# Kernel optimization log

Measured on AMD Instinct MI355X. Metric: run time of the kernel, lower is better.

The kernel has to match this reference:

```python
import jax, jax.numpy as jnp
import numpy as np

N_NODES = 50000
N_EDGES = 800000
D = 128
R = 8


def setup_inputs() -> dict:
    key = jax.random.key(0)
    ks = jax.random.split(key, 8)
    x = jax.random.normal(ks[0], (N_NODES, D), dtype=jnp.float32)
    edge_index = jax.random.randint(ks[1], (2, N_EDGES), 0, N_NODES, dtype=jnp.int64)
    edge_type = jax.random.randint(ks[2], (N_EDGES,), 0, R, dtype=jnp.int64)
    scale = 0.02
    W1 = jax.random.normal(ks[3], (R, D, D), dtype=jnp.float32) * scale
    root1 = jax.random.normal(ks[4], (D, D), dtype=jnp.float32) * scale
    b1 = jnp.zeros((D,), dtype=jnp.float32)
    W2 = jax.random.normal(ks[5], (R, D, D), dtype=jnp.float32) * scale
    root2 = jax.random.normal(ks[6], (D, D), dtype=jnp.float32) * scale
    b2 = jnp.zeros((D,), dtype=jnp.float32)
    return {"x": x, "edge_index": edge_index, "edge_type": edge_type,
            "W1": W1, "root1": root1, "b1": b1,
            "W2": W2, "root2": root2, "b2": b2}


def rgcn_conv(x, src, dst, etype, W, root, b):
    """PyG RGCNConv: per-relation mean aggregation + root transform + bias."""
    n = x.shape[0]
    out = x @ root + b  # [N, O]
    num_rel = W.shape[0]
    for r in range(num_rel):  # small fixed relation count
        m = (etype == r).astype(x.dtype)  # [E] relation mask as weight
        y = x @ W[r]  # [N, O] transform once per relation
        msg = y[src] * m[:, None]  # [E, O] gathered, masked messages
        s = jax.ops.segment_sum(msg, dst, num_segments=n)
        cnt = jax.ops.segment_sum(m, dst, num_segments=n)
        out = out + s / jnp.clip(cnt, 1.0)[:, None]
    return out


def reference(x, edge_index, edge_type, W1, root1, b1, W2, root2, b2):
    src, dst = edge_index[0], edge_index[1]
    h = rgcn_conv(x, src, dst, edge_type, W1, root1, b1)
    h = jax.nn.relu(h)
    h = rgcn_conv(h, src, dst, edge_type, W2, root2, b2)
    # F.normalize(h, dim=-1): x / max(||x||_2, eps)
    norm = jnp.linalg.norm(h, axis=-1, keepdims=True)
    return h / jnp.maximum(norm, 1e-12)
```

## Files before the change

### kernel.cpp

```cpp
#include <hip/hip_runtime.h>

#define NN 50000
#define NE 800000
#define DD 128
#define RR 8
#define MB (NN * RR)
#define SCAN_BLK 2048
#define NBLK ((MB + SCAN_BLK - 1) / SCAN_BLK)

typedef __attribute__((ext_vector_type(8))) short short8;
typedef __attribute__((ext_vector_type(4))) float f32x4;

__device__ __forceinline__ unsigned short f2bf(float f)
{
    unsigned int u = __float_as_uint(f);
    u = (u + 0x7FFFu + ((u >> 16) & 1u)) >> 16;
    return (unsigned short)u;
}
__device__ __forceinline__ float bflo(unsigned int p) { return __uint_as_float(p << 16); }
__device__ __forceinline__ float bfhi(unsigned int p) { return __uint_as_float(p & 0xFFFF0000u); }

__global__ __launch_bounds__(256) void k_count(const int* __restrict__ ei,
                                               const int* __restrict__ et,
                                               int* __restrict__ cnt)
{
    int e = blockIdx.x * 256 + threadIdx.x;
    if (e < NE) {
        int r = et[e];
        int dst = ei[NE + e];
        atomicAdd(&cnt[r * NN + dst], 1);
    }
}

__global__ __launch_bounds__(256) void k_scan1(const int* __restrict__ cnt,
                                               int* __restrict__ off,
                                               int* __restrict__ bsum)
{
    __shared__ int lds[256];
    int t = threadIdx.x;
    int base = blockIdx.x * SCAN_BLK + t * 8;
    int v[8], s = 0;
    #pragma unroll
    for (int j = 0; j < 8; j++) {
        int idx = base + j;
        v[j] = (idx < MB) ? cnt[idx] : 0;
        s += v[j];
    }
    lds[t] = s;
    __syncthreads();
    for (int d = 1; d < 256; d <<= 1) {
        int u = (t >= d) ? lds[t - d] : 0;
        __syncthreads();
        lds[t] += u;
        __syncthreads();
    }
    if (t == 255) bsum[blockIdx.x] = lds[255];
    int run = lds[t] - s;
    #pragma unroll
    for (int j = 0; j < 8; j++) {
        int idx = base + j;
        if (idx < MB) off[idx] = run;
        run += v[j];
    }
}

__global__ __launch_bounds__(256) void k_scan2(const int* __restrict__ bsum,
                                               int* __restrict__ carry)
{
    __shared__ int lds[256];
    int t = threadIdx.x;
    int s = (t < NBLK) ? bsum[t] : 0;
    lds[t] = s;
    __syncthreads();
    for (int d = 1; d < 256; d <<= 1) {
        int u = (t >= d) ? lds[t - d] : 0;
        __syncthreads();
        lds[t] += u;
        __syncthreads();
    }
    if (t < NBLK) carry[t] = lds[t] - s;
}

__global__ __launch_bounds__(256) void k_scan3(int* __restrict__ off,
                                               const int* __restrict__ carry)
{
    int c = carry[blockIdx.x];
    int base = blockIdx.x * SCAN_BLK + threadIdx.x * 8;
    #pragma unroll
    for (int j = 0; j < 8; j++) {
        int idx = base + j;
        if (idx < MB) off[idx] += c;
    }
    if (blockIdx.x == 0 && threadIdx.x == 0) off[MB] = NE;
}

__global__ __launch_bounds__(256) void k_place(const int* __restrict__ ei,
                                               const int* __restrict__ et,
                                               const int* __restrict__ off,
                                               int* __restrict__ fill,
                                               int* __restrict__ srt)
{
    int e = blockIdx.x * 256 + threadIdx.x;
    if (e < NE) {
        int r = et[e];
        int src = ei[e];
        int dst = ei[NE + e];
        int b = r * NN + dst;
        int pos = off[b] + atomicAdd(&fill[b], 1);
        srt[pos] = src;
    }
}

__global__ __launch_bounds__(256) void k_tobf16(const float* __restrict__ x,
                                                unsigned short* __restrict__ xb, int n4)
{
    int i = blockIdx.x * 256 + threadIdx.x;
    if (i < n4) {
        float4 v = ((const float4*)x)[i];
        uint2 o;
        o.x = (unsigned int)f2bf(v.x) | ((unsigned int)f2bf(v.y) << 16);
        o.y = (unsigned int)f2bf(v.z) | ((unsigned int)f2bf(v.w) << 16);
        ((uint2*)xb)[i] = o;
    }
}

__global__ __launch_bounds__(256) void k_wconv(const float* __restrict__ W1,
                                               const float* __restrict__ root1,
                                               const float* __restrict__ W2,
                                               const float* __restrict__ root2,
                                               unsigned short* __restrict__ Wb)
{
    int e = blockIdx.x * 256 + threadIdx.x;
    if (e >= 18 * 16384) return;
    int m = e >> 14;
    int rem = e & 16383;
    int n = rem >> 7;
    int k = rem & 127;
    float v;
    if (m < 8)       v = W1[m * 16384 + k * 128 + n];
    else if (m == 8) v = root1[k * 128 + n];
    else if (m < 17) v = W2[(m - 9) * 16384 + k * 128 + n];
    else             v = root2[k * 128 + n];
    Wb[e] = f2bf(v);
}

__global__ __launch_bounds__(512) void k_layer(const unsigned short* __restrict__ Xin,
                                               const unsigned short* __restrict__ Wb,
                                               const float* __restrict__ bias,
                                               const int* __restrict__ off,
                                               const int* __restrict__ srt,
                                               unsigned short* __restrict__ out_bf,
                                               float* __restrict__ out_f,
                                               int mode)
{
    __shared__ unsigned short Wl[128 * 128];
    __shared__ unsigned short Al[64 * 128];
    const int t = threadIdx.x;
    const int w = t >> 6;
    const int lane = t & 63;
    const int grow0 = blockIdx.x * 64;
    const int colb = lane & 15;
    const int hi = lane >> 4;
    const int g = t >> 4;
    const int l16 = t & 15;

    const int arow = ((w >> 1) << 4) + colb;
    const int aswz = (arow & 7) << 4;

    f32x4 acc[4];
    #pragma unroll
    for (int tt = 0; tt < 4; tt++) acc[tt] = f32x4{0.f, 0.f, 0.f, 0.f};

    for (int m = 0; m < 9; m++) {
        {
            const uint4* wsrc = (const uint4*)(Wb + (size_t)m * 16384);
            #pragma unroll
            for (int c = 0; c < 4; c++) {
                int u = c * 512 + t;
                uint4 v = wsrc[u];
                int n = u >> 4;
                int dstb = (u * 16) ^ ((n & 7) << 4);
                *(uint4*)((char*)Wl + dstb) = v;
            }
        }
        if (m < 8) {
            int b0 = m * NN + grow0;
            #pragma unroll
            for (int rr = 0; rr < 2; rr++) {
                int row = g * 2 + rr;
                int dstn = grow0 + row;
                float a0 = 0.f, a1 = 0.f, a2 = 0.f, a3 = 0.f;
                float a4 = 0.f, a5 = 0.f, a6 = 0.f, a7 = 0.f;
                int c = 0;
                if (dstn < NN) {
                    int s0 = off[b0 + row];
                    int s1 = off[b0 + row + 1];
                    c = s1 - s0;
                    for (int k = 0; k < c; k++) {
                        int src = srt[s0 + k];
                        uint4 u = *(const uint4*)(Xin + (size_t)src * 128 + l16 * 8);
                        a0 += bflo(u.x); a1 += bfhi(u.x);
                        a2 += bflo(u.y); a3 += bfhi(u.y);
                        a4 += bflo(u.z); a5 += bfhi(u.z);
                        a6 += bflo(u.w); a7 += bfhi(u.w);
                    }
                }
                float invc = 1.0f / (float)(c > 1 ? c : 1);
                uint4 o;
                o.x = (unsigned int)f2bf(a0 * invc) | ((unsigned int)f2bf(a1 * invc) << 16);
                o.y = (unsigned int)f2bf(a2 * invc) | ((unsigned int)f2bf(a3 * invc) << 16);
                o.z = (unsigned int)f2bf(a4 * invc) | ((unsigned int)f2bf(a5 * invc) << 16);
                o.w = (unsigned int)f2bf(a6 * invc) | ((unsigned int)f2bf(a7 * invc) << 16);
                int byteoff = (row * 256 + l16 * 16) ^ ((row & 7) << 4);
                *(uint4*)((char*)Al + byteoff) = o;
            }
        }
        __syncthreads();

        if (m < 8) {
            #pragma unroll
            for (int ks = 0; ks < 4; ks++) {
                int abyte = (arow * 256 + ks * 64 + hi * 16) ^ aswz;
                short8 af = *(const short8*)((const char*)Al + abyte);
                #pragma unroll
                for (int tt = 0; tt < 4; tt++) {
                    int n = (w & 1) * 64 + tt * 16 + colb;
                    int bbyte = (n * 256 + ks * 64 + hi * 16) ^ ((n & 7) << 4);
                    short8 bfr = *(const short8*)((const char*)Wl + bbyte);
                    acc[tt] = __builtin_amdgcn_mfma_f32_16x16x32_bf16(af, bfr, acc[tt], 0, 0, 0);
                }
            }
        } else {
            int rowg = grow0 + arow;
            #pragma unroll
            for (int ks = 0; ks < 4; ks++) {
                short8 af = short8{0,0,0,0,0,0,0,0};
                if (rowg < NN)
                    af = *(const short8*)(Xin + (size_t)rowg * 128 + ks * 32 + hi * 8);
                #pragma unroll
                for (int tt = 0; tt < 4; tt++) {
                    int n = (w & 1) * 64 + tt * 16 + colb;
                    int bbyte = (n * 256 + ks * 64 + hi * 16) ^ ((n & 7) << 4);
                    short8 bfr = *(const short8*)((const char*)Wl + bbyte);
                    acc[tt] = __builtin_amdgcn_mfma_f32_16x16x32_bf16(af, bfr, acc[tt], 0, 0, 0);
                }
            }
        }
        __syncthreads();
    }

    const int rl_base = (w >> 1) << 4;
    if (mode == 0) {
        #pragma unroll
        for (int tt = 0; tt < 4; tt++) {
            int col = (w & 1) * 64 + tt * 16 + colb;
            float bc = bias[col];
            #pragma unroll
            for (int j = 0; j < 4; j++) {
                int row = grow0 + rl_base + hi * 4 + j;
                if (row < NN) {
                    float v = fmaxf(acc[tt][j] + bc, 0.f);
                    out_bf[(size_t)row * 128 + col] = f2bf(v);
                }
            }
        }
    } else {
        float vv[4][4];
        float ss[4] = {0.f, 0.f, 0.f, 0.f};
        #pragma unroll
        for (int tt = 0; tt < 4; tt++) {
            int col = (w & 1) * 64 + tt * 16 + colb;
            float bc = bias[col];
            #pragma unroll
            for (int j = 0; j < 4; j++) {
                float v = acc[tt][j] + bc;
                vv[tt][j] = v;
                ss[j] += v * v;
            }
        }
        #pragma unroll
        for (int j = 0; j < 4; j++) {
            #pragma unroll
            for (int o = 1; o < 16; o <<= 1) ss[j] += __shfl_xor(ss[j], o);
        }
        float* nrm = (float*)Al;
        if (colb == 0) {
            #pragma unroll
            for (int j = 0; j < 4; j++) nrm[(rl_base + hi * 4 + j) * 2 + (w & 1)] = ss[j];
        }
        __syncthreads();
        #pragma unroll
        for (int tt = 0; tt < 4; tt++) {
            int col = (w & 1) * 64 + tt * 16 + colb;
            #pragma unroll
            for (int j = 0; j < 4; j++) {
                int rl = rl_base + hi * 4 + j;
                int row = grow0 + rl;
                if (row < NN) {
                    float tot = nrm[rl * 2] + nrm[rl * 2 + 1];
                    float inv = 1.0f / fmaxf(sqrtf(tot), 1e-12f);
                    out_f[(size_t)row * 128 + col] = vv[tt][j] * inv;
                }
            }
        }
    }
}

extern "C" void kernel_launch(void* const* d_in, const int* in_sizes, int n_in,
                              void* d_out, int out_size, void* d_ws, size_t ws_size,
                              hipStream_t stream)
{
    const float* x     = (const float*)d_in[0];
    const int*   ei    = (const int*)d_in[1];
    const int*   et    = (const int*)d_in[2];
    const float* W1    = (const float*)d_in[3];
    const float* root1 = (const float*)d_in[4];
    const float* b1    = (const float*)d_in[5];
    const float* W2    = (const float*)d_in[6];
    const float* root2 = (const float*)d_in[7];
    const float* b2    = (const float*)d_in[8];
    float* out = (float*)d_out;

    char* ws = (char*)d_ws;
    int* cnt   = (int*)ws;
    int* fill  = cnt + MB;
    int* off   = fill + MB;
    int* bsum  = off + MB + 1;
    int* carry = bsum + 256;
    int* srt   = carry + 256;
    unsigned short* Xb = (unsigned short*)(srt + NE);
    unsigned short* hb = Xb + (size_t)NN * DD;
    unsigned short* Wb = hb + (size_t)NN * DD;

    hipMemsetAsync(cnt, 0, (size_t)2 * MB * 4, stream);

    k_count<<<(NE + 255) / 256, 256, 0, stream>>>(ei, et, cnt);
    k_scan1<<<NBLK, 256, 0, stream>>>(cnt, off, bsum);
    k_scan2<<<1, 256, 0, stream>>>(bsum, carry);
    k_scan3<<<NBLK, 256, 0, stream>>>(off, carry);
    k_place<<<(NE + 255) / 256, 256, 0, stream>>>(ei, et, off, fill, srt);

    k_tobf16<<<(NN * DD / 4 + 255) / 256, 256, 0, stream>>>(x, Xb, NN * DD / 4);
    k_wconv<<<(18 * 16384 + 255) / 256, 256, 0, stream>>>(W1, root1, W2, root2, Wb);

    int lay_grid = (NN + 63) / 64;
    k_layer<<<lay_grid, 512, 0, stream>>>(Xb, Wb, b1, off, srt, hb, nullptr, 0);
    k_layer<<<lay_grid, 512, 0, stream>>>(hb, Wb + (size_t)9 * 16384, b2, off, srt, nullptr, out, 1);
}
```

Measured before the change: 379.2 us.

## Hoist all-relation neighbor gather before GEMM loop with 32-row tiles

The layer kernel now gathers and sums neighbor features for all 8 relations up front into registers (64 floats per thread), with the loads unrolled by two. The gather no longer sits between weight staging and MFMA inside each relation iteration. The row tile shrinks from 64 to 32 so each thread handles one destination row. Each wave now covers 16 rows by 32 columns, and the grid doubles. The aim is more memory-level parallelism in the random gathers and fewer sync-serialized gather phases. The cost is higher register pressure, and each block reloads the 9 weight matrices for only 32 rows, doubling LDS weight traffic per row.

```diff
diff --git a/kernel.cpp b/kernel.cpp
--- a/kernel.cpp
+++ b/kernel.cpp
@@ -154,23 +154,69 @@
                                                int mode)
 {
     __shared__ unsigned short Wl[128 * 128];
-    __shared__ unsigned short Al[64 * 128];
+    __shared__ unsigned short Al[32 * 128];
     const int t = threadIdx.x;
     const int w = t >> 6;
     const int lane = t & 63;
-    const int grow0 = blockIdx.x * 64;
+    const int grow0 = blockIdx.x * 32;
     const int colb = lane & 15;
     const int hi = lane >> 4;
     const int g = t >> 4;
     const int l16 = t & 15;
 
-    const int arow = ((w >> 1) << 4) + colb;
+    const int rt = w & 1;
+    const int ct0 = w >> 1;
+    const int arow = rt * 16 + colb;
     const int aswz = (arow & 7) << 4;
 
-    f32x4 acc[4];
-    #pragma unroll
-    for (int tt = 0; tt < 4; tt++) acc[tt] = f32x4{0.f, 0.f, 0.f, 0.f};
-
+    float a[8][8];
+    #pragma unroll
+    for (int m = 0; m < 8; m++)
+        #pragma unroll
+        for (int j = 0; j < 8; j++) a[m][j] = 0.f;
+    int cdeg[8];
+    #pragma unroll
+    for (int m = 0; m < 8; m++) cdeg[m] = 0;
+
+    int row = grow0 + g;
+    if (row < NN) {
+        int s_[8], e_[8];
+        #pragma unroll
+        for (int m = 0; m < 8; m++) s_[m] = off[m * NN + row];
+        #pragma unroll
+        for (int m = 0; m < 8; m++) e_[m] = off[m * NN + row + 1];
+        #pragma unroll
+        for (int m = 0; m < 8; m++) {
+            int s = s_[m];
+            int c = e_[m] - s;
+            cdeg[m] = c;
+            int k = 0;
+            for (; k + 2 <= c; k += 2) {
+                int p0 = srt[s + k];
+                int p1 = srt[s + k + 1];
+                uint4 u0 = *(const uint4*)(Xin + (size_t)p0 * 128 + l16 * 8);
+                uint4 u1 = *(const uint4*)(Xin + (size_t)p1 * 128 + l16 * 8);
+                a[m][0] += bflo(u0.x) + bflo(u1.x); a[m][1] += bfhi(u0.x) + bfhi(u1.x);
+                a[m][2] += bflo(u0.y) + bflo(u1.y); a[m][3] += bfhi(u0.y) + bfhi(u1.y);
+                a[m][4] += bflo(u0.z) + bflo(u1.z); a[m][5] += bfhi(u0.z) + bfhi(u1.z);
+                a[m][6] += bflo(u0.w) + bflo(u1.w); a[m][7] += bfhi(u0.w) + bfhi(u1.w);
+            }
+            if (k < c) {
+                int p0 = srt[s + k];
+                uint4 u0 = *(const uint4*)(Xin + (size_t)p0 * 128 + l16 * 8);
+                a[m][0] += bflo(u0.x); a[m][1] += bfhi(u0.x);
+                a[m][2] += bflo(u0.y); a[m][3] += bfhi(u0.y);
+                a[m][4] += bflo(u0.z); a[m][5] += bfhi(u0.z);
+                a[m][6] += bflo(u0.w); a[m][7] += bfhi(u0.w);
+            }
+        }
+    }
+
+    f32x4 acc[2];
+    acc[0] = f32x4{0.f, 0.f, 0.f, 0.f};
+    acc[1] = f32x4{0.f, 0.f, 0.f, 0.f};
+
+    #pragma unroll
     for (int m = 0; m < 9; m++) {
         {
             const uint4* wsrc = (const uint4*)(Wb + (size_t)m * 16384);
@@ -184,36 +230,14 @@
             }
         }
         if (m < 8) {
-            int b0 = m * NN + grow0;
-            #pragma unroll
-            for (int rr = 0; rr < 2; rr++) {
-                int row = g * 2 + rr;
-                int dstn = grow0 + row;
-                float a0 = 0.f, a1 = 0.f, a2 = 0.f, a3 = 0.f;
-                float a4 = 0.f, a5 = 0.f, a6 = 0.f, a7 = 0.f;
-                int c = 0;
-                if (dstn < NN) {
-                    int s0 = off[b0 + row];
-                    int s1 = off[b0 + row + 1];
-                    c = s1 - s0;
-                    for (int k = 0; k < c; k++) {
-                        int src = srt[s0 + k];
-                        uint4 u = *(const uint4*)(Xin + (size_t)src * 128 + l16 * 8);
-                        a0 += bflo(u.x); a1 += bfhi(u.x);
-                        a2 += bflo(u.y); a3 += bfhi(u.y);
-                        a4 += bflo(u.z); a5 += bfhi(u.z);
-                        a6 += bflo(u.w); a7 += bfhi(u.w);
-                    }
-                }
-                float invc = 1.0f / (float)(c > 1 ? c : 1);
-                uint4 o;
-                o.x = (unsigned int)f2bf(a0 * invc) | ((unsigned int)f2bf(a1 * invc) << 16);
-                o.y = (unsigned int)f2bf(a2 * invc) | ((unsigned int)f2bf(a3 * invc) << 16);
-                o.z = (unsigned int)f2bf(a4 * invc) | ((unsigned int)f2bf(a5 * invc) << 16);
-                o.w = (unsigned int)f2bf(a6 * invc) | ((unsigned int)f2bf(a7 * invc) << 16);
-                int byteoff = (row * 256 + l16 * 16) ^ ((row & 7) << 4);
-                *(uint4*)((char*)Al + byteoff) = o;
-            }
+            float invc = 1.0f / (float)(cdeg[m] > 1 ? cdeg[m] : 1);
+            uint4 o;
+            o.x = (unsigned int)f2bf(a[m][0] * invc) | ((unsigned int)f2bf(a[m][1] * invc) << 16);
+            o.y = (unsigned int)f2bf(a[m][2] * invc) | ((unsigned int)f2bf(a[m][3] * invc) << 16);
+            o.z = (unsigned int)f2bf(a[m][4] * invc) | ((unsigned int)f2bf(a[m][5] * invc) << 16);
+            o.w = (unsigned int)f2bf(a[m][6] * invc) | ((unsigned int)f2bf(a[m][7] * invc) << 16);
+            int byteoff = (g * 256 + l16 * 16) ^ ((g & 7) << 4);
+            *(uint4*)((char*)Al + byteoff) = o;
         }
         __syncthreads();
 
@@ -223,11 +247,11 @@
                 int abyte = (arow * 256 + ks * 64 + hi * 16) ^ aswz;
                 short8 af = *(const short8*)((const char*)Al + abyte);
                 #pragma unroll
-                for (int tt = 0; tt < 4; tt++) {
-                    int n = (w & 1) * 64 + tt * 16 + colb;
+                for (int tti = 0; tti < 2; tti++) {
+                    int n = (ct0 + tti * 4) * 16 + colb;
                     int bbyte = (n * 256 + ks * 64 + hi * 16) ^ ((n & 7) << 4);
                     short8 bfr = *(const short8*)((const char*)Wl + bbyte);
-                    acc[tt] = __builtin_amdgcn_mfma_f32_16x16x32_bf16(af, bfr, acc[tt], 0, 0, 0);
+                    acc[tti] = __builtin_amdgcn_mfma_f32_16x16x32_bf16(af, bfr, acc[tti], 0, 0, 0);
                 }
             }
         } else {
@@ -238,43 +262,42 @@
                 if (rowg < NN)
                     af = *(const short8*)(Xin + (size_t)rowg * 128 + ks * 32 + hi * 8);
                 #pragma unroll
-                for (int tt = 0; tt < 4; tt++) {
-                    int n = (w & 1) * 64 + tt * 16 + colb;
+                for (int tti = 0; tti < 2; tti++) {
+                    int n = (ct0 + tti * 4) * 16 + colb;
                     int bbyte = (n * 256 + ks * 64 + hi * 16) ^ ((n & 7) << 4);
                     short8 bfr = *(const short8*)((const char*)Wl + bbyte);
-                    acc[tt] = __builtin_amdgcn_mfma_f32_16x16x32_bf16(af, bfr, acc[tt], 0, 0, 0);
+                    acc[tti] = __builtin_amdgcn_mfma_f32_16x16x32_bf16(af, bfr, acc[tti], 0, 0, 0);
                 }
             }
         }
         __syncthreads();
     }
 
-    const int rl_base = (w >> 1) << 4;
     if (mode == 0) {
         #pragma unroll
-        for (int tt = 0; tt < 4; tt++) {
-            int col = (w & 1) * 64 + tt * 16 + colb;
+        for (int tti = 0; tti < 2; tti++) {
+            int col = (ct0 + tti * 4) * 16 + colb;
             float bc = bias[col];
             #pragma unroll
             for (int j = 0; j < 4; j++) {
-                int row = grow0 + rl_base + hi * 4 + j;
-                if (row < NN) {
-                    float v = fmaxf(acc[tt][j] + bc, 0.f);
-                    out_bf[(size_t)row * 128 + col] = f2bf(v);
+                int rowg = grow0 + rt * 16 + hi * 4 + j;
+                if (rowg < NN) {
+                    float v = fmaxf(acc[tti][j] + bc, 0.f);
+                    out_bf[(size_t)rowg * 128 + col] = f2bf(v);
                 }
             }
         }
     } else {
-        float vv[4][4];
+        float vv[2][4];
         float ss[4] = {0.f, 0.f, 0.f, 0.f};
         #pragma unroll
-        for (int tt = 0; tt < 4; tt++) {
-            int col = (w & 1) * 64 + tt * 16 + colb;
+        for (int tti = 0; tti < 2; tti++) {
+            int col = (ct0 + tti * 4) * 16 + colb;
             float bc = bias[col];
             #pragma unroll
             for (int j = 0; j < 4; j++) {
-                float v = acc[tt][j] + bc;
-                vv[tt][j] = v;
+                float v = acc[tti][j] + bc;
+                vv[tti][j] = v;
                 ss[j] += v * v;
             }
         }
@@ -286,20 +309,20 @@
         float* nrm = (float*)Al;
         if (colb == 0) {
             #pragma unroll
-            for (int j = 0; j < 4; j++) nrm[(rl_base + hi * 4 + j) * 2 + (w & 1)] = ss[j];
-        }
-        __syncthreads();
-        #pragma unroll
-        for (int tt = 0; tt < 4; tt++) {
-            int col = (w & 1) * 64 + tt * 16 + colb;
+            for (int j = 0; j < 4; j++) nrm[(rt * 16 + hi * 4 + j) * 4 + ct0] = ss[j];
+        }
+        __syncthreads();
+        #pragma unroll
+        for (int tti = 0; tti < 2; tti++) {
+            int col = (ct0 + tti * 4) * 16 + colb;
             #pragma unroll
             for (int j = 0; j < 4; j++) {
-                int rl = rl_base + hi * 4 + j;
-                int row = grow0 + rl;
-                if (row < NN) {
-                    float tot = nrm[rl * 2] + nrm[rl * 2 + 1];
+                int rl = rt * 16 + hi * 4 + j;
+                int rowg = grow0 + rl;
+                if (rowg < NN) {
+                    float tot = nrm[rl * 4] + nrm[rl * 4 + 1] + nrm[rl * 4 + 2] + nrm[rl * 4 + 3];
                     float inv = 1.0f / fmaxf(sqrtf(tot), 1e-12f);
-                    out_f[(size_t)row * 128 + col] = vv[tt][j] * inv;
+                    out_f[(size_t)rowg * 128 + col] = vv[tti][j] * inv;
                 }
             }
         }
@@ -343,7 +366,7 @@
     k_tobf16<<<(NN * DD / 4 + 255) / 256, 256, 0, stream>>>(x, Xb, NN * DD / 4);
     k_wconv<<<(18 * 16384 + 255) / 256, 256, 0, stream>>>(W1, root1, W2, root2, Wb);
 
-    int lay_grid = (NN + 63) / 64;
+    int lay_grid = (NN + 31) / 32;
     k_layer<<<lay_grid, 512, 0, stream>>>(Xb, Wb, b1, off, srt, hb, nullptr, 0);
     k_layer<<<lay_grid, 512, 0, stream>>>(hb, Wb + (size_t)9 * 16384, b2, off, srt, nullptr, out, 1);
 }
```

Measured after the change: 322.4 us. -15.0%, faster.
